# Kernel tuning notes

Measured on AMD Instinct MI355X. Metric: run time of the kernel, lower is better.

## Reference

```python
import jax, jax.numpy as jnp
import numpy as np

N = 50000   # nodes
E = 600000  # edges (avg degree ~12)
R = 8       # num_relations = 2 * n_speakers**2, n_speakers=2
B = 32      # num_bases = args.batch_size
GD, H1, H2 = 128, 128, 128


def setup_inputs() -> dict:
    key = jax.random.key(0)
    ks = jax.random.split(key, 16)
    w = lambda k, shape: jax.random.normal(k, shape, jnp.float32) * 0.05
    return {
        "node_features": jax.random.normal(ks[0], (N, GD), jnp.float32),
        "edge_index": jax.random.randint(ks[1], (2, E), 0, N),
        "edge_norm": jax.random.uniform(ks[2], (E,), jnp.float32),
        "edge_type": jax.random.randint(ks[3], (E,), 0, R),
        "basis": w(ks[4], (B, GD, H1)),
        "comp": w(ks[5], (R, B)),
        "root": w(ks[6], (GD, H1)),
        "bias1": jnp.zeros((H1,), jnp.float32),
        "w_key": w(ks[7], (H1, H2)),
        "b_key": jnp.zeros((H2,), jnp.float32),
        "w_query": w(ks[8], (H1, H2)),
        "b_query": jnp.zeros((H2,), jnp.float32),
        "w_value": w(ks[9], (H1, H2)),
        "b_value": jnp.zeros((H2,), jnp.float32),
        "w_skip": w(ks[10], (H1, H2)),
        "b_skip": jnp.zeros((H2,), jnp.float32),
    }


def reference(node_features, edge_index, edge_norm, edge_type, basis, comp,
              root, bias1, w_key, b_key, w_query, b_query, w_value, b_value,
              w_skip, b_skip):
    n = node_features.shape[0]
    r = comp.shape[0]
    src, dst = edge_index[0], edge_index[1]

    # ---- RGCNConv (basis decomposition, per-relation mean aggregation) ----
    W = jnp.einsum('rb,bio->rio', comp, basis)            # [R, GD, H1]
    xW = jnp.einsum('ni,rio->rno', node_features, W)      # [R, N, H1]
    msg = xW[edge_type, src]                              # [E, H1]
    seg = edge_type * n + dst                             # combined (relation, dst) segment id
    agg = jax.ops.segment_sum(msg, seg, num_segments=r * n).reshape(r, n, -1)
    cnt = jax.ops.segment_sum(jnp.ones(msg.shape[0], jnp.float32), seg,
                              num_segments=r * n).reshape(r, n, 1)
    h = (agg / jnp.maximum(cnt, 1.0)).sum(0) + node_features @ root + bias1

    # ---- ResGatedGraphConv: sigmoid(k_i + q_j) * v_j, sum-aggregated + skip ----
    k = h @ w_key + b_key
    q = h @ w_query + b_query
    v = h @ w_value + b_value
    m = jax.nn.sigmoid(k[dst] + q[src]) * v[src]          # [E, H2]
    out = jax.ops.segment_sum(m, dst, num_segments=n) + h @ w_skip + b_skip
    return out
```

## Files before the change

kernel.cpp:

```cpp
#include <hip/hip_runtime.h>
#include <stdint.h>

#define GD 128
#define H1 128
#define H2 128
#define NBASES 32
#define NREL 8
#define KZ 1152

typedef __attribute__((ext_vector_type(8))) short bf16x8;
typedef __attribute__((ext_vector_type(4))) float f32x4;

static inline size_t align256(size_t x){ return (x + 255) & ~(size_t)255; }

__device__ __forceinline__ float bf2f(uint32_t u16){
  union { uint32_t u; float f; } c; c.u = (u16 & 0xffffu) << 16; return c.f;
}
__device__ __forceinline__ unsigned short f2bf(float f){
  union { float f; uint32_t u; } c; c.f = f;
  uint32_t u = c.u;
  u += 0x7fffu + ((u >> 16) & 1u);
  return (unsigned short)(u >> 16);
}
__device__ __forceinline__ uint32_t pkbf(float a, float b){
  union { float f; uint32_t u; } ca, cb; ca.f = a; cb.f = b;
  return __builtin_amdgcn_perm(cb.u + 0x8000u, ca.u + 0x8000u, 0x07060302u);
}

__device__ __forceinline__ void async_copy16(void* lds_dst, const void* gsrc){
  __builtin_amdgcn_global_load_lds(
      (const __attribute__((address_space(1))) uint32_t*)gsrc,
      (__attribute__((address_space(3))) uint32_t*)lds_dst, 16, 0, 0);
}

__global__ void k_prep(const float* __restrict__ comp, const float* __restrict__ basis,
                       const float* __restrict__ root, unsigned short* __restrict__ Bz,
                       const float* __restrict__ wk, const float* __restrict__ wq,
                       const float* __restrict__ wv, const float* __restrict__ wsk,
                       const float* __restrict__ bk, const float* __restrict__ bq,
                       const float* __restrict__ bv, const float* __restrict__ bs,
                       unsigned short* __restrict__ B2t, float* __restrict__ Bb,
                       const float4* __restrict__ x, uint2* __restrict__ xout, int cnt4,
                       uint32_t* __restrict__ xpadz, int npadz,
                       const int* __restrict__ edst, const int* __restrict__ etyp,
                       int* __restrict__ cnt, int E, int n){
  int b = blockIdx.x, t = threadIdx.x;
  if (b < 576){
    int idx = b*256 + t;
    int row = idx >> 7, i = idx & 127;
    int r = row >> 7, o = row & 127;
    float v;
    if (r < 8){
      float acc = 0.f;
      #pragma unroll
      for (int bb = 0; bb < NBASES; ++bb)
        acc += comp[r*NBASES + bb] * basis[((size_t)bb*GD + i)*H1 + o];
      v = acc;
    } else {
      v = root[(size_t)i*H1 + o];
    }
    Bz[idx] = f2bf(v);
  } else if (b < 576 + 256){
    int idx = (b - 576)*256 + t;
    int c = idx / H1, k = idx % H1;
    const float* w = (c < 128) ? wk : (c < 256) ? wq : (c < 384) ? wv : wsk;
    B2t[idx] = f2bf(w[(size_t)k*H2 + (c & 127)]);
    if (idx < 512){
      const float* bia = (idx < 128) ? bk : (idx < 256) ? bq : (idx < 384) ? bv : bs;
      Bb[idx] = bia[idx & 127];
    }
  } else {
    int cb = b - (576 + 256);
    int ncastb = (cnt4 + 255) >> 8;
    if (cb < ncastb){
      int i = cb*256 + t;
      if (i < cnt4){
        float4 v = x[i];
        uint2 o; o.x = pkbf(v.x, v.y); o.y = pkbf(v.z, v.w);
        xout[i] = o;
      }
    } else if (cb < ncastb + 12){
      int i = (cb - ncastb)*256 + t;
      if (i < npadz) xpadz[i] = 0u;
    } else {
      int e = (cb - ncastb - 12)*256 + t;
      if (e < E) atomicAdd(&cnt[etyp[e]*n + edst[e]], 1);
    }
  }
}

__global__ void k_scanA(const int* __restrict__ deg, int* __restrict__ off,
                        int* __restrict__ btot, int len){
  __shared__ int wsum[16];
  int t = threadIdx.x, lane = t & 63, w = t >> 6;
  int i0 = blockIdx.x*8192 + t*8;
  int v[8];
  if (i0 + 7 < len){
    int4 va = *(const int4*)(deg + i0);
    int4 vb = *(const int4*)(deg + i0 + 4);
    v[0]=va.x; v[1]=va.y; v[2]=va.z; v[3]=va.w;
    v[4]=vb.x; v[5]=vb.y; v[6]=vb.z; v[7]=vb.w;
  } else {
    #pragma unroll
    for (int u = 0; u < 8; ++u) v[u] = (i0+u < len) ? deg[i0+u] : 0;
  }
  int s[8]; s[0] = v[0];
  #pragma unroll
  for (int u = 1; u < 8; ++u) s[u] = s[u-1] + v[u];
  int x = s[7];
  #pragma unroll
  for (int d = 1; d < 64; d <<= 1){
    int u = __shfl_up(x, d, 64);
    if (lane >= d) x += u;
  }
  if (lane == 63) wsum[w] = x;
  __syncthreads();
  if (t < 16){
    int y = wsum[t];
    #pragma unroll
    for (int d = 1; d < 16; d <<= 1){
      int u = __shfl_up(y, d, 16);
      if (t >= d) y += u;
    }
    wsum[t] = y;
  }
  __syncthreads();
  int woff = (w > 0) ? wsum[w-1] : 0;
  int excl = woff + x - s[7];
  #pragma unroll
  for (int u = 0; u < 8; ++u)
    if (i0+u < len) off[i0+u] = excl + s[u] - v[u];
  if (t == 0) btot[blockIdx.x] = wsum[15];
}

__global__ void k_scanB(const int* __restrict__ btot, int* __restrict__ off,
                        int* __restrict__ cursor, int len, int sentinel){
  int t = threadIdx.x, bid = blockIdx.x;
  int add = 0;
  for (int j = 0; j < bid; ++j) add += btot[j];
  int i0 = bid*8192 + t*8;
  #pragma unroll
  for (int u = 0; u < 8; ++u){
    int i = i0 + u;
    if (i < len){ int val = off[i] + add; off[i] = val; cursor[i] = val; }
  }
  if (bid == 0 && t == 0) off[len] = sentinel;
}

__global__ void k_scatter_rd(const int* __restrict__ src, const int* __restrict__ dst,
                             const int* __restrict__ typ, int* __restrict__ cursor,
                             int* __restrict__ pk, int E, int n){
  int e = blockIdx.x*blockDim.x + threadIdx.x;
  if (e >= E) return;
  int pos = atomicAdd(&cursor[typ[e]*n + dst[e]], 1);
  pk[pos] = src[e];
}

__launch_bounds__(256)
__global__ void k_zgemm(const unsigned short* __restrict__ A, const unsigned short* __restrict__ Bt,
                        unsigned short* __restrict__ Z){
  __shared__ char lds[16384];
  int t = threadIdx.x, lane = t & 63, wave = t >> 6;
  int row0 = blockIdx.x * 128;
  int c0 = blockIdx.y * 128;
  int mrow = lane & 15, quad = lane >> 4;
  int wrow = (wave & 1) * 64, wcol = (wave >> 1) * 64;
  int s = (mrow >> 1) & 3;

  const unsigned short* Asrc = A + (size_t)(row0 + (t >> 2))*H1 + (((t & 3) ^ ((t >> 3) & 3)) << 3);
  const unsigned short* Bsrc = Bt + (size_t)(c0 + (t >> 2))*H1 + (((t & 3) ^ ((t >> 3) & 3)) << 3);
  char* ldsw = lds + wave*1024;

  int aoff = (wrow + mrow)*64 + ((quad ^ s) << 4);
  int boff = 8192 + (wcol + mrow)*64 + ((quad ^ s) << 4);

  f32x4 acc[4][4];
  #pragma unroll
  for (int i = 0; i < 4; ++i)
    #pragma unroll
    for (int j = 0; j < 4; ++j) acc[i][j] = (f32x4){0.f,0.f,0.f,0.f};

  #pragma unroll
  for (int kt = 0; kt < H1; kt += 32){
    __syncthreads();
    async_copy16(ldsw,         Asrc + kt);
    async_copy16(ldsw + 4096,  Asrc + (size_t)64*H1 + kt);
    async_copy16(ldsw + 8192,  Bsrc + kt);
    async_copy16(ldsw + 12288, Bsrc + (size_t)64*H1 + kt);
    __syncthreads();
    bf16x8 af[4], bf[4];
    #pragma unroll
    for (int i = 0; i < 4; ++i) af[i] = *(const bf16x8*)(lds + aoff + i*1024);
    #pragma unroll
    for (int j = 0; j < 4; ++j) bf[j] = *(const bf16x8*)(lds + boff + j*1024);
    #pragma unroll
    for (int i = 0; i < 4; ++i)
      #pragma unroll
      for (int j = 0; j < 4; ++j)
        acc[i][j] = __builtin_amdgcn_mfma_f32_16x16x32_bf16(af[i], bf[j], acc[i][j], 0, 0, 0);
  }
  #pragma unroll
  for (int j = 0; j < 4; ++j){
    int col = c0 + wcol + j*16 + mrow;
    #pragma unroll
    for (int i = 0; i < 4; ++i)
      #pragma unroll
      for (int rg = 0; rg < 4; ++rg){
        int row = row0 + wrow + i*16 + quad*4 + rg;
        Z[(size_t)row*KZ + col] = f2bf(acc[i][j][rg]);
      }
  }
}

__global__ void k_edge1(const int* __restrict__ off_rd, const int* __restrict__ pk_rd,
                        const unsigned short* __restrict__ Zb,
                        const float* __restrict__ bias1,
                        unsigned short* __restrict__ h, int n, int npad){
  int wid = blockIdx.x*(blockDim.x >> 6) + (threadIdx.x >> 6);
  int lane = threadIdx.x & 63;
  if (wid >= npad) return;
  uint32_t* hrow = (uint32_t*)(h + (size_t)wid*H1);
  if (wid >= n){ hrow[lane] = 0u; return; }
  const uint32_t* Z32 = (const uint32_t*)Zb;
  int r8 = lane & 7;
  int o_r = off_rd[(size_t)r8*n + wid];
  int e_r = off_rd[(size_t)r8*n + wid + 1];
  int c_r = e_r - o_r;
  float ic_r = (c_r > 0) ? (1.f/(float)c_r) : 0.f;
  int c0_ = __builtin_amdgcn_readlane(c_r, 0), c1_ = __builtin_amdgcn_readlane(c_r, 1);
  int c2_ = __builtin_amdgcn_readlane(c_r, 2), c3_ = __builtin_amdgcn_readlane(c_r, 3);
  int c4_ = __builtin_amdgcn_readlane(c_r, 4), c5_ = __builtin_amdgcn_readlane(c_r, 5);
  int c6_ = __builtin_amdgcn_readlane(c_r, 6), c7_ = __builtin_amdgcn_readlane(c_r, 7);
  int o0_ = __builtin_amdgcn_readlane(o_r, 0), o1_ = __builtin_amdgcn_readlane(o_r, 1);
  int o2_ = __builtin_amdgcn_readlane(o_r, 2), o3_ = __builtin_amdgcn_readlane(o_r, 3);
  int o4_ = __builtin_amdgcn_readlane(o_r, 4), o5_ = __builtin_amdgcn_readlane(o_r, 5);
  int o6_ = __builtin_amdgcn_readlane(o_r, 6), o7_ = __builtin_amdgcn_readlane(o_r, 7);
  float i0f = __int_as_float(__builtin_amdgcn_readlane(__float_as_int(ic_r), 0));
  float i1f = __int_as_float(__builtin_amdgcn_readlane(__float_as_int(ic_r), 1));
  float i2f = __int_as_float(__builtin_amdgcn_readlane(__float_as_int(ic_r), 2));
  float i3f = __int_as_float(__builtin_amdgcn_readlane(__float_as_int(ic_r), 3));
  float i4f = __int_as_float(__builtin_amdgcn_readlane(__float_as_int(ic_r), 4));
  float i5f = __int_as_float(__builtin_amdgcn_readlane(__float_as_int(ic_r), 5));
  float i6f = __int_as_float(__builtin_amdgcn_readlane(__float_as_int(ic_r), 6));
  float i7f = __int_as_float(__builtin_amdgcn_readlane(__float_as_int(ic_r), 7));
  int p1 = c0_, p2 = p1 + c1_, p3 = p2 + c2_, p4 = p3 + c3_;
  int p5 = p4 + c4_, p6 = p5 + c5_, p7 = p6 + c6_, dg = p7 + c7_;

  float a0 = 0.f, a1 = 0.f;
  for (int jb = 0; jb < dg; jb += 64){
    int i = jb + lane;
    int adj = o0_, rel = 0;
    float wv = i0f;
    adj = (i >= p1) ? (o1_ - p1) : adj;  rel += (i >= p1);  wv = (i >= p1) ? i1f : wv;
    adj = (i >= p2) ? (o2_ - p2) : adj;  rel += (i >= p2);  wv = (i >= p2) ? i2f : wv;
    adj = (i >= p3) ? (o3_ - p3) : adj;  rel += (i >= p3);  wv = (i >= p3) ? i3f : wv;
    adj = (i >= p4) ? (o4_ - p4) : adj;  rel += (i >= p4);  wv = (i >= p4) ? i4f : wv;
    adj = (i >= p5) ? (o5_ - p5) : adj;  rel += (i >= p5);  wv = (i >= p5) ? i5f : wv;
    adj = (i >= p6) ? (o6_ - p6) : adj;  rel += (i >= p6);  wv = (i >= p6) ? i6f : wv;
    adj = (i >= p7) ? (o7_ - p7) : adj;  rel += (i >= p7);  wv = (i >= p7) ? i7f : wv;
    int m = dg - jb; if (m > 64) m = 64;
    int pj = (lane < m) ? pk_rd[adj + i] : 0;
    int gidx = pj*(KZ/2) + rel*64;
    int jj = 0;
    for (; jj + 8 <= m; jj += 8){
      uint32_t g[8]; float wgt[8];
      #pragma unroll
      for (int k = 0; k < 8; ++k){
        int gx = __builtin_amdgcn_readlane(gidx, jj + k);
        wgt[k] = __int_as_float(__builtin_amdgcn_readlane(__float_as_int(wv), jj + k));
        g[k] = Z32[(size_t)(uint32_t)gx + lane];
      }
      #pragma unroll
      for (int k = 0; k < 8; ++k){
        a0 += bf2f(g[k]) * wgt[k];
        a1 += bf2f(g[k] >> 16) * wgt[k];
      }
    }
    for (; jj + 4 <= m; jj += 4){
      uint32_t g[4]; float wgt[4];
      #pragma unroll
      for (int k = 0; k < 4; ++k){
        int gx = __builtin_amdgcn_readlane(gidx, jj + k);
        wgt[k] = __int_as_float(__builtin_amdgcn_readlane(__float_as_int(wv), jj + k));
        g[k] = Z32[(size_t)(uint32_t)gx + lane];
      }
      #pragma unroll
      for (int k = 0; k < 4; ++k){
        a0 += bf2f(g[k]) * wgt[k];
        a1 += bf2f(g[k] >> 16) * wgt[k];
      }
    }
    for (; jj < m; ++jj){
      int gx = __builtin_amdgcn_readlane(gidx, jj);
      float wg = __int_as_float(__builtin_amdgcn_readlane(__float_as_int(wv), jj));
      uint32_t gg = Z32[(size_t)(uint32_t)gx + lane];
      a0 += bf2f(gg) * wg;
      a1 += bf2f(gg >> 16) * wg;
    }
  }
  uint32_t zr = Z32[(size_t)wid*(KZ/2) + 512 + lane];
  float2 bb = ((const float2*)bias1)[lane];
  hrow[lane] = pkbf(a0 + bf2f(zr) + bb.x, a1 + bf2f(zr >> 16) + bb.y);
}

__launch_bounds__(256)
__global__ void k_gemm2(const unsigned short* __restrict__ A, const unsigned short* __restrict__ Bt,
                        const float* __restrict__ Bb, unsigned short* __restrict__ kqv,
                        unsigned short* __restrict__ skipb, int n){
  __shared__ char lds[16384];
  int t = threadIdx.x, lane = t & 63, wave = t >> 6;
  int row0 = blockIdx.x * 128;
  int c0 = blockIdx.y * 128;
  int mrow = lane & 15, quad = lane >> 4;
  int wrow = (wave & 1) * 64, wcol = (wave >> 1) * 64;
  int s = (mrow >> 1) & 3;

  const unsigned short* Asrc = A + (size_t)(row0 + (t >> 2))*H1 + (((t & 3) ^ ((t >> 3) & 3)) << 3);
  const unsigned short* Bsrc = Bt + (size_t)(c0 + (t >> 2))*H1 + (((t & 3) ^ ((t >> 3) & 3)) << 3);
  char* ldsw = lds + wave*1024;

  int aoff = (wrow + mrow)*64 + ((quad ^ s) << 4);
  int boff = 8192 + (wcol + mrow)*64 + ((quad ^ s) << 4);

  f32x4 acc[4][4];
  #pragma unroll
  for (int i = 0; i < 4; ++i)
    #pragma unroll
    for (int j = 0; j < 4; ++j) acc[i][j] = (f32x4){0.f,0.f,0.f,0.f};

  #pragma unroll
  for (int kt = 0; kt < H1; kt += 32){
    __syncthreads();
    async_copy16(ldsw,         Asrc + kt);
    async_copy16(ldsw + 4096,  Asrc + (size_t)64*H1 + kt);
    async_copy16(ldsw + 8192,  Bsrc + kt);
    async_copy16(ldsw + 12288, Bsrc + (size_t)64*H1 + kt);
    __syncthreads();
    bf16x8 af[4], bf[4];
    #pragma unroll
    for (int i = 0; i < 4; ++i) af[i] = *(const bf16x8*)(lds + aoff + i*1024);
    #pragma unroll
    for (int j = 0; j < 4; ++j) bf[j] = *(const bf16x8*)(lds + boff + j*1024);
    #pragma unroll
    for (int i = 0; i < 4; ++i)
      #pragma unroll
      for (int j = 0; j < 4; ++j)
        acc[i][j] = __builtin_amdgcn_mfma_f32_16x16x32_bf16(af[i], bf[j], acc[i][j], 0, 0, 0);
  }
  #pragma unroll
  for (int j = 0; j < 4; ++j){
    int col = c0 + wcol + j*16 + mrow;
    float bcol = Bb[col];
    #pragma unroll
    for (int i = 0; i < 4; ++i)
      #pragma unroll
      for (int rg = 0; rg < 4; ++rg){
        int rr = row0 + wrow + i*16 + quad*4 + rg;
        if (rr >= n) continue;
        float v = acc[i][j][rg] + bcol;
        if (col < 128){
          kqv[(size_t)rr*384 + col] = f2bf(v);
        } else if (col < 256){
          int jj = col - 128;
          kqv[(size_t)rr*384 + 128 + ((jj >> 1) << 2) + (jj & 1)] = f2bf(v);
        } else if (col < 384){
          int jj = col - 256;
          kqv[(size_t)rr*384 + 128 + ((jj >> 1) << 2) + 2 + (jj & 1)] = f2bf(v);
        } else {
          skipb[(size_t)rr*H2 + (col - 384)] = f2bf(v);
        }
      }
  }
}

__global__ void k_edge2(const int* __restrict__ off_rd, const int* __restrict__ pk_rd,
                        const unsigned short* __restrict__ kqv,
                        const unsigned short* __restrict__ skipb,
                        float* __restrict__ out, int n){
  int wid = blockIdx.x*(blockDim.x >> 6) + (threadIdx.x >> 6);
  int lane = threadIdx.x & 63;
  if (wid >= n) return;
  const uint32_t* kv32 = (const uint32_t*)kqv;
  int r = lane & 7;
  int o_r = off_rd[(size_t)r*n + wid];
  int e_r = off_rd[(size_t)r*n + wid + 1];
  int c_r = e_r - o_r;
  int c0_ = __builtin_amdgcn_readlane(c_r, 0), c1_ = __builtin_amdgcn_readlane(c_r, 1);
  int c2_ = __builtin_amdgcn_readlane(c_r, 2), c3_ = __builtin_amdgcn_readlane(c_r, 3);
  int c4_ = __builtin_amdgcn_readlane(c_r, 4), c5_ = __builtin_amdgcn_readlane(c_r, 5);
  int c6_ = __builtin_amdgcn_readlane(c_r, 6), c7_ = __builtin_amdgcn_readlane(c_r, 7);
  int o0_ = __builtin_amdgcn_readlane(o_r, 0), o1_ = __builtin_amdgcn_readlane(o_r, 1);
  int o2_ = __builtin_amdgcn_readlane(o_r, 2), o3_ = __builtin_amdgcn_readlane(o_r, 3);
  int o4_ = __builtin_amdgcn_readlane(o_r, 4), o5_ = __builtin_amdgcn_readlane(o_r, 5);
  int o6_ = __builtin_amdgcn_readlane(o_r, 6), o7_ = __builtin_amdgcn_readlane(o_r, 7);
  int p1 = c0_, p2 = p1 + c1_, p3 = p2 + c2_, p4 = p3 + c3_;
  int p5 = p4 + c4_, p6 = p5 + c5_, p7 = p6 + c6_, dg = p7 + c7_;

  uint32_t ku = kv32[(size_t)wid*192 + lane];
  float k0 = bf2f(ku), k1 = bf2f(ku >> 16);
  float a0 = 0.f, a1 = 0.f;
  for (int jb = 0; jb < dg; jb += 64){
    int i = jb + lane;
    int adj = o0_;
    adj = (i >= p1) ? (o1_ - p1) : adj;
    adj = (i >= p2) ? (o2_ - p2) : adj;
    adj = (i >= p3) ? (o3_ - p3) : adj;
    adj = (i >= p4) ? (o4_ - p4) : adj;
    adj = (i >= p5) ? (o5_ - p5) : adj;
    adj = (i >= p6) ? (o6_ - p6) : adj;
    adj = (i >= p7) ? (o7_ - p7) : adj;
    int m = dg - jb; if (m > 64) m = 64;
    int pj = (lane < m) ? pk_rd[adj + i] : 0;
    int jj = 0;
    for (; jj + 8 <= m; jj += 8){
      uint2 q[8];
      #pragma unroll
      for (int k = 0; k < 8; ++k){
        int s = __builtin_amdgcn_readlane(pj, jj + k);
        q[k] = *(const uint2*)(kv32 + (size_t)s*192 + 64 + lane*2);
      }
      #pragma unroll
      for (int k = 0; k < 8; ++k){
        float qq0 = bf2f(q[k].x), qq1 = bf2f(q[k].x >> 16);
        float vv0 = bf2f(q[k].y), vv1 = bf2f(q[k].y >> 16);
        float g0 = 1.f / (1.f + __expf(-(k0 + qq0)));
        float g1 = 1.f / (1.f + __expf(-(k1 + qq1)));
        a0 += g0*vv0; a1 += g1*vv1;
      }
    }
    for (; jj + 4 <= m; jj += 4){
      uint2 q[4];
      #pragma unroll
      for (int k = 0; k < 4; ++k){
        int s = __builtin_amdgcn_readlane(pj, jj + k);
        q[k] = *(const uint2*)(kv32 + (size_t)s*192 + 64 + lane*2);
      }
      #pragma unroll
      for (int k = 0; k < 4; ++k){
        float qq0 = bf2f(q[k].x), qq1 = bf2f(q[k].x >> 16);
        float vv0 = bf2f(q[k].y), vv1 = bf2f(q[k].y >> 16);
        float g0 = 1.f / (1.f + __expf(-(k0 + qq0)));
        float g1 = 1.f / (1.f + __expf(-(k1 + qq1)));
        a0 += g0*vv0; a1 += g1*vv1;
      }
    }
    for (; jj < m; ++jj){
      int s = __builtin_amdgcn_readlane(pj, jj);
      uint2 qc = *(const uint2*)(kv32 + (size_t)s*192 + 64 + lane*2);
      float qq0 = bf2f(qc.x), qq1 = bf2f(qc.x >> 16);
      float vv0 = bf2f(qc.y), vv1 = bf2f(qc.y >> 16);
      float g0 = 1.f / (1.f + __expf(-(k0 + qq0)));
      float g1 = 1.f / (1.f + __expf(-(k1 + qq1)));
      a0 += g0*vv0; a1 += g1*vv1;
    }
  }
  uint32_t sk = ((const uint32_t*)skipb)[(size_t)wid*64 + lane];
  float2 cur; cur.x = a0 + bf2f(sk); cur.y = a1 + bf2f(sk >> 16);
  ((float2*)(out + (size_t)wid*H2))[lane] = cur;
}

extern "C" void kernel_launch(void* const* d_in, const int* in_sizes, int n_in,
                              void* d_out, int out_size, void* d_ws, size_t ws_size,
                              hipStream_t stream){
  const float* x     = (const float*)d_in[0];
  const int*   eidx  = (const int*)  d_in[1];
  const int*   etype = (const int*)  d_in[3];
  const float* basis = (const float*)d_in[4];
  const float* comp  = (const float*)d_in[5];
  const float* root  = (const float*)d_in[6];
  const float* bias1 = (const float*)d_in[7];
  const float* wk    = (const float*)d_in[8];
  const float* bk    = (const float*)d_in[9];
  const float* wq    = (const float*)d_in[10];
  const float* bq    = (const float*)d_in[11];
  const float* wv    = (const float*)d_in[12];
  const float* bv    = (const float*)d_in[13];
  const float* wsk   = (const float*)d_in[14];
  const float* bs    = (const float*)d_in[15];
  const int n = in_sizes[0] / GD;
  const int E = in_sizes[3];
  const int npad = (n + 127) & ~127;
  const int* esrc = eidx;
  const int* edst = eidx + E;
  float* out = (float*)d_out;

  char* w = (char*)d_ws;
  size_t off = 0;
  unsigned short* xbf  = (unsigned short*)(w + off); off = align256(off + (size_t)npad*GD*2);
  unsigned short* Zbuf = (unsigned short*)(w + off); off = align256(off + (size_t)npad*KZ*2);
  unsigned short* Bz   = (unsigned short*)(w + off); off = align256(off + (size_t)KZ*H1*2);
  unsigned short* B2t  = (unsigned short*)(w + off); off = align256(off + (size_t)512*H1*2);
  float* Bb            = (float*)(w + off);          off = align256(off + 512*4);
  unsigned short* hbuf = (unsigned short*)(w + off); off = align256(off + (size_t)npad*H1*2);
  unsigned short* kqv  = (unsigned short*)(w + off); off = align256(off + (size_t)n*384*2);
  unsigned short* skipb= (unsigned short*)(w + off); off = align256(off + (size_t)npad*H2*2);
  int* cnt_rd          = (int*)(w + off);            off = align256(off + (size_t)(8*n+4)*4);
  int* off_rd          = (int*)(w + off);            off = align256(off + (size_t)(8*n+1)*4);
  int* cur_rd          = (int*)(w + off);            off = align256(off + (size_t)8*n*4);
  int* btot_rd         = (int*)(w + off);            off = align256(off + 64*4);
  int* pk_rd           = (int*)(w + off);            off = align256(off + (size_t)E*4);

  const int nblk_rd = (8*n + 8191) / 8192;
  const int cnt4 = n*GD/4;
  const int ncastb = (cnt4 + 255)/256;
  const int histb  = (E + 255)/256;
  const int npadz  = (npad - n)*GD/2;

  hipMemsetAsync(cnt_rd, 0, (size_t)8*n*4, stream);

  k_prep<<<576 + 256 + ncastb + 12 + histb, 256, 0, stream>>>(
      comp, basis, root, Bz, wk, wq, wv, wsk, bk, bq, bv, bs, B2t, Bb,
      (const float4*)x, (uint2*)xbf, cnt4,
      (uint32_t*)(xbf + (size_t)n*GD), npadz,
      edst, etype, cnt_rd, E, n);
  k_scanA<<<nblk_rd, 1024, 0, stream>>>(cnt_rd, off_rd, btot_rd, 8*n);
  k_scanB<<<nblk_rd, 1024, 0, stream>>>(btot_rd, off_rd, cur_rd, 8*n, E);
  k_scatter_rd<<<(E + 255)/256, 256, 0, stream>>>(esrc, edst, etype, cur_rd, pk_rd, E, n);
  k_zgemm<<<dim3(npad/128, KZ/128), 256, 0, stream>>>(xbf, Bz, Zbuf);
  k_edge1<<<(npad + 3)/4, 256, 0, stream>>>(off_rd, pk_rd, Zbuf, bias1, hbuf, n, npad);
  k_gemm2<<<dim3(npad/128, 4), 256, 0, stream>>>(hbuf, B2t, Bb, kqv, skipb, n);
  k_edge2<<<(n + 3)/4, 256, 0, stream>>>(off_rd, pk_rd, kqv, skipb, out, n);
}
```

Measured before the change: 379.2 us.

## Replace relation-by-destination CSR with destination-only CSR packing relation in index

Builds a CSR keyed only by destination node instead of by (relation, destination), with the edge's relation packed into the high bits of the source index. The scan shrinks from 8n to n entries and becomes a single-block serial-carry scan, so one kernel launch is removed. Per-relation counts are now recomputed inside edge1 with wave ballots instead of being read from eight offset arrays. The tradeoff is a single-block scan over n entries and extra ballot work per node. It also assumes node ids fit in 20 bits.

New measurement: 411.9 us. +8.6%, slower.

```diff
diff --git a/kernel.cpp b/kernel.cpp
--- a/kernel.cpp
+++ b/kernel.cpp
@@ -42,8 +42,7 @@
                        unsigned short* __restrict__ B2t, float* __restrict__ Bb,
                        const float4* __restrict__ x, uint2* __restrict__ xout, int cnt4,
                        uint32_t* __restrict__ xpadz, int npadz,
-                       const int* __restrict__ edst, const int* __restrict__ etyp,
-                       int* __restrict__ cnt, int E, int n){
+                       const int* __restrict__ edst, int* __restrict__ cnt, int E){
   int b = blockIdx.x, t = threadIdx.x;
   if (b < 576){
     int idx = b*256 + t;
@@ -84,76 +83,74 @@
       if (i < npadz) xpadz[i] = 0u;
     } else {
       int e = (cb - ncastb - 12)*256 + t;
-      if (e < E) atomicAdd(&cnt[etyp[e]*n + edst[e]], 1);
-    }
-  }
-}
-
-__global__ void k_scanA(const int* __restrict__ deg, int* __restrict__ off,
-                        int* __restrict__ btot, int len){
+      if (e < E) atomicAdd(&cnt[edst[e]], 1);
+    }
+  }
+}
+
+__global__ void k_scan1(const int* __restrict__ deg, int* __restrict__ off,
+                        int* __restrict__ cursor, int n, int E){
   __shared__ int wsum[16];
+  __shared__ int carry_s;
   int t = threadIdx.x, lane = t & 63, w = t >> 6;
-  int i0 = blockIdx.x*8192 + t*8;
-  int v[8];
-  if (i0 + 7 < len){
-    int4 va = *(const int4*)(deg + i0);
-    int4 vb = *(const int4*)(deg + i0 + 4);
-    v[0]=va.x; v[1]=va.y; v[2]=va.z; v[3]=va.w;
-    v[4]=vb.x; v[5]=vb.y; v[6]=vb.z; v[7]=vb.w;
-  } else {
-    #pragma unroll
-    for (int u = 0; u < 8; ++u) v[u] = (i0+u < len) ? deg[i0+u] : 0;
-  }
-  int s[8]; s[0] = v[0];
-  #pragma unroll
-  for (int u = 1; u < 8; ++u) s[u] = s[u-1] + v[u];
-  int x = s[7];
-  #pragma unroll
-  for (int d = 1; d < 64; d <<= 1){
-    int u = __shfl_up(x, d, 64);
-    if (lane >= d) x += u;
-  }
-  if (lane == 63) wsum[w] = x;
+  if (t == 0) carry_s = 0;
   __syncthreads();
-  if (t < 16){
-    int y = wsum[t];
-    #pragma unroll
-    for (int d = 1; d < 16; d <<= 1){
-      int u = __shfl_up(y, d, 16);
-      if (t >= d) y += u;
-    }
-    wsum[t] = y;
-  }
-  __syncthreads();
-  int woff = (w > 0) ? wsum[w-1] : 0;
-  int excl = woff + x - s[7];
-  #pragma unroll
-  for (int u = 0; u < 8; ++u)
-    if (i0+u < len) off[i0+u] = excl + s[u] - v[u];
-  if (t == 0) btot[blockIdx.x] = wsum[15];
-}
-
-__global__ void k_scanB(const int* __restrict__ btot, int* __restrict__ off,
-                        int* __restrict__ cursor, int len, int sentinel){
-  int t = threadIdx.x, bid = blockIdx.x;
-  int add = 0;
-  for (int j = 0; j < bid; ++j) add += btot[j];
-  int i0 = bid*8192 + t*8;
-  #pragma unroll
-  for (int u = 0; u < 8; ++u){
-    int i = i0 + u;
-    if (i < len){ int val = off[i] + add; off[i] = val; cursor[i] = val; }
-  }
-  if (bid == 0 && t == 0) off[len] = sentinel;
-}
-
-__global__ void k_scatter_rd(const int* __restrict__ src, const int* __restrict__ dst,
-                             const int* __restrict__ typ, int* __restrict__ cursor,
-                             int* __restrict__ pk, int E, int n){
+  for (int base = 0; base < n; base += 8192){
+    int i0 = base + t*8;
+    int v[8];
+    if (i0 + 7 < n){
+      int4 va = *(const int4*)(deg + i0);
+      int4 vb = *(const int4*)(deg + i0 + 4);
+      v[0]=va.x; v[1]=va.y; v[2]=va.z; v[3]=va.w;
+      v[4]=vb.x; v[5]=vb.y; v[6]=vb.z; v[7]=vb.w;
+    } else {
+      #pragma unroll
+      for (int u = 0; u < 8; ++u) v[u] = (i0+u < n) ? deg[i0+u] : 0;
+    }
+    int s[8]; s[0] = v[0];
+    #pragma unroll
+    for (int u = 1; u < 8; ++u) s[u] = s[u-1] + v[u];
+    int x = s[7];
+    #pragma unroll
+    for (int d = 1; d < 64; d <<= 1){
+      int u = __shfl_up(x, d, 64);
+      if (lane >= d) x += u;
+    }
+    if (lane == 63) wsum[w] = x;
+    int carry = carry_s;
+    __syncthreads();
+    if (t < 16){
+      int y = wsum[t];
+      #pragma unroll
+      for (int d = 1; d < 16; d <<= 1){
+        int u = __shfl_up(y, d, 16);
+        if (t >= d) y += u;
+      }
+      wsum[t] = y;
+    }
+    __syncthreads();
+    int woff = (w > 0) ? wsum[w-1] : 0;
+    int total = wsum[15];
+    int excl = carry + woff + x - s[7];
+    #pragma unroll
+    for (int u = 0; u < 8; ++u){
+      int i = i0 + u;
+      if (i < n){ int val = excl + s[u] - v[u]; off[i] = val; cursor[i] = val; }
+    }
+    __syncthreads();
+    if (t == 0) carry_s = carry + total;
+    __syncthreads();
+  }
+  if (t == 0) off[n] = E;
+}
+
+__global__ void k_scatter_d(const int* __restrict__ src, const int* __restrict__ dst,
+                            const int* __restrict__ typ, int* __restrict__ cursor,
+                            int* __restrict__ pk, int E){
   int e = blockIdx.x*blockDim.x + threadIdx.x;
   if (e >= E) return;
-  int pos = atomicAdd(&cursor[typ[e]*n + dst[e]], 1);
-  pk[pos] = src[e];
+  int pos = atomicAdd(&cursor[dst[e]], 1);
+  pk[pos] = src[e] | (typ[e] << 20);
 }
 
 __launch_bounds__(256)
@@ -212,7 +209,7 @@
   }
 }
 
-__global__ void k_edge1(const int* __restrict__ off_rd, const int* __restrict__ pk_rd,
+__global__ void k_edge1(const int* __restrict__ off_d, const int* __restrict__ pk_d,
                         const unsigned short* __restrict__ Zb,
                         const float* __restrict__ bias1,
                         unsigned short* __restrict__ h, int n, int npad){
@@ -222,45 +219,26 @@
   uint32_t* hrow = (uint32_t*)(h + (size_t)wid*H1);
   if (wid >= n){ hrow[lane] = 0u; return; }
   const uint32_t* Z32 = (const uint32_t*)Zb;
-  int r8 = lane & 7;
-  int o_r = off_rd[(size_t)r8*n + wid];
-  int e_r = off_rd[(size_t)r8*n + wid + 1];
-  int c_r = e_r - o_r;
-  float ic_r = (c_r > 0) ? (1.f/(float)c_r) : 0.f;
-  int c0_ = __builtin_amdgcn_readlane(c_r, 0), c1_ = __builtin_amdgcn_readlane(c_r, 1);
-  int c2_ = __builtin_amdgcn_readlane(c_r, 2), c3_ = __builtin_amdgcn_readlane(c_r, 3);
-  int c4_ = __builtin_amdgcn_readlane(c_r, 4), c5_ = __builtin_amdgcn_readlane(c_r, 5);
-  int c6_ = __builtin_amdgcn_readlane(c_r, 6), c7_ = __builtin_amdgcn_readlane(c_r, 7);
-  int o0_ = __builtin_amdgcn_readlane(o_r, 0), o1_ = __builtin_amdgcn_readlane(o_r, 1);
-  int o2_ = __builtin_amdgcn_readlane(o_r, 2), o3_ = __builtin_amdgcn_readlane(o_r, 3);
-  int o4_ = __builtin_amdgcn_readlane(o_r, 4), o5_ = __builtin_amdgcn_readlane(o_r, 5);
-  int o6_ = __builtin_amdgcn_readlane(o_r, 6), o7_ = __builtin_amdgcn_readlane(o_r, 7);
-  float i0f = __int_as_float(__builtin_amdgcn_readlane(__float_as_int(ic_r), 0));
-  float i1f = __int_as_float(__builtin_amdgcn_readlane(__float_as_int(ic_r), 1));
-  float i2f = __int_as_float(__builtin_amdgcn_readlane(__float_as_int(ic_r), 2));
-  float i3f = __int_as_float(__builtin_amdgcn_readlane(__float_as_int(ic_r), 3));
-  float i4f = __int_as_float(__builtin_amdgcn_readlane(__float_as_int(ic_r), 4));
-  float i5f = __int_as_float(__builtin_amdgcn_readlane(__float_as_int(ic_r), 5));
-  float i6f = __int_as_float(__builtin_amdgcn_readlane(__float_as_int(ic_r), 6));
-  float i7f = __int_as_float(__builtin_amdgcn_readlane(__float_as_int(ic_r), 7));
-  int p1 = c0_, p2 = p1 + c1_, p3 = p2 + c2_, p4 = p3 + c3_;
-  int p5 = p4 + c4_, p6 = p5 + c5_, p7 = p6 + c6_, dg = p7 + c7_;
+  int ov = off_d[wid + (lane & 1)];
+  int o = __builtin_amdgcn_readlane(ov, 0);
+  int dg = __builtin_amdgcn_readlane(ov, 1) - o;
 
   float a0 = 0.f, a1 = 0.f;
-  for (int jb = 0; jb < dg; jb += 64){
-    int i = jb + lane;
-    int adj = o0_, rel = 0;
-    float wv = i0f;
-    adj = (i >= p1) ? (o1_ - p1) : adj;  rel += (i >= p1);  wv = (i >= p1) ? i1f : wv;
-    adj = (i >= p2) ? (o2_ - p2) : adj;  rel += (i >= p2);  wv = (i >= p2) ? i2f : wv;
-    adj = (i >= p3) ? (o3_ - p3) : adj;  rel += (i >= p3);  wv = (i >= p3) ? i3f : wv;
-    adj = (i >= p4) ? (o4_ - p4) : adj;  rel += (i >= p4);  wv = (i >= p4) ? i4f : wv;
-    adj = (i >= p5) ? (o5_ - p5) : adj;  rel += (i >= p5);  wv = (i >= p5) ? i5f : wv;
-    adj = (i >= p6) ? (o6_ - p6) : adj;  rel += (i >= p6);  wv = (i >= p6) ? i6f : wv;
-    adj = (i >= p7) ? (o7_ - p7) : adj;  rel += (i >= p7);  wv = (i >= p7) ? i7f : wv;
-    int m = dg - jb; if (m > 64) m = 64;
-    int pj = (lane < m) ? pk_rd[adj + i] : 0;
-    int gidx = pj*(KZ/2) + rel*64;
+  if (dg <= 64){
+    int m = dg;
+    int pj = (lane < m) ? pk_d[o + lane] : 0;
+    int rel = (pj >> 20) & 7;
+    int cr[8];
+    #pragma unroll
+    for (int r = 0; r < 8; ++r)
+      cr[r] = __popcll(__ballot(lane < m && rel == r));
+    float inv[8];
+    #pragma unroll
+    for (int r = 0; r < 8; ++r) inv[r] = (cr[r] > 0) ? 1.f/(float)cr[r] : 0.f;
+    float wv = inv[0];
+    #pragma unroll
+    for (int r = 1; r < 8; ++r) wv = (rel == r) ? inv[r] : wv;
+    int gidx = (pj & 0xFFFFF)*(KZ/2) + rel*64;
     int jj = 0;
     for (; jj + 8 <= m; jj += 8){
       uint32_t g[8]; float wgt[8];
@@ -296,6 +274,52 @@
       uint32_t gg = Z32[(size_t)(uint32_t)gx + lane];
       a0 += bf2f(gg) * wg;
       a1 += bf2f(gg >> 16) * wg;
+    }
+  } else {
+    int cr[8];
+    #pragma unroll
+    for (int r = 0; r < 8; ++r) cr[r] = 0;
+    for (int jb = 0; jb < dg; jb += 64){
+      int m = dg - jb; if (m > 64) m = 64;
+      int pj = (lane < m) ? pk_d[o + jb + lane] : 0;
+      int rel = (pj >> 20) & 7;
+      #pragma unroll
+      for (int r = 0; r < 8; ++r)
+        cr[r] += __popcll(__ballot(lane < m && rel == r));
+    }
+    float inv[8];
+    #pragma unroll
+    for (int r = 0; r < 8; ++r) inv[r] = (cr[r] > 0) ? 1.f/(float)cr[r] : 0.f;
+    for (int jb = 0; jb < dg; jb += 64){
+      int m = dg - jb; if (m > 64) m = 64;
+      int pj = (lane < m) ? pk_d[o + jb + lane] : 0;
+      int rel = (pj >> 20) & 7;
+      float wv = inv[0];
+      #pragma unroll
+      for (int r = 1; r < 8; ++r) wv = (rel == r) ? inv[r] : wv;
+      int gidx = (pj & 0xFFFFF)*(KZ/2) + rel*64;
+      int jj = 0;
+      for (; jj + 8 <= m; jj += 8){
+        uint32_t g[8]; float wgt[8];
+        #pragma unroll
+        for (int k = 0; k < 8; ++k){
+          int gx = __builtin_amdgcn_readlane(gidx, jj + k);
+          wgt[k] = __int_as_float(__builtin_amdgcn_readlane(__float_as_int(wv), jj + k));
+          g[k] = Z32[(size_t)(uint32_t)gx + lane];
+        }
+        #pragma unroll
+        for (int k = 0; k < 8; ++k){
+          a0 += bf2f(g[k]) * wgt[k];
+          a1 += bf2f(g[k] >> 16) * wgt[k];
+        }
+      }
+      for (; jj < m; ++jj){
+        int gx = __builtin_amdgcn_readlane(gidx, jj);
+        float wg = __int_as_float(__builtin_amdgcn_readlane(__float_as_int(wv), jj));
+        uint32_t gg = Z32[(size_t)(uint32_t)gx + lane];
+        a0 += bf2f(gg) * wg;
+        a1 += bf2f(gg >> 16) * wg;
+      }
     }
   }
   uint32_t zr = Z32[(size_t)wid*(KZ/2) + 512 + lane];
@@ -373,7 +397,7 @@
   }
 }
 
-__global__ void k_edge2(const int* __restrict__ off_rd, const int* __restrict__ pk_rd,
+__global__ void k_edge2(const int* __restrict__ off_d, const int* __restrict__ pk_d,
                         const unsigned short* __restrict__ kqv,
                         const unsigned short* __restrict__ skipb,
                         float* __restrict__ out, int n){
@@ -381,42 +405,22 @@
   int lane = threadIdx.x & 63;
   if (wid >= n) return;
   const uint32_t* kv32 = (const uint32_t*)kqv;
-  int r = lane & 7;
-  int o_r = off_rd[(size_t)r*n + wid];
-  int e_r = off_rd[(size_t)r*n + wid + 1];
-  int c_r = e_r - o_r;
-  int c0_ = __builtin_amdgcn_readlane(c_r, 0), c1_ = __builtin_amdgcn_readlane(c_r, 1);
-  int c2_ = __builtin_amdgcn_readlane(c_r, 2), c3_ = __builtin_amdgcn_readlane(c_r, 3);
-  int c4_ = __builtin_amdgcn_readlane(c_r, 4), c5_ = __builtin_amdgcn_readlane(c_r, 5);
-  int c6_ = __builtin_amdgcn_readlane(c_r, 6), c7_ = __builtin_amdgcn_readlane(c_r, 7);
-  int o0_ = __builtin_amdgcn_readlane(o_r, 0), o1_ = __builtin_amdgcn_readlane(o_r, 1);
-  int o2_ = __builtin_amdgcn_readlane(o_r, 2), o3_ = __builtin_amdgcn_readlane(o_r, 3);
-  int o4_ = __builtin_amdgcn_readlane(o_r, 4), o5_ = __builtin_amdgcn_readlane(o_r, 5);
-  int o6_ = __builtin_amdgcn_readlane(o_r, 6), o7_ = __builtin_amdgcn_readlane(o_r, 7);
-  int p1 = c0_, p2 = p1 + c1_, p3 = p2 + c2_, p4 = p3 + c3_;
-  int p5 = p4 + c4_, p6 = p5 + c5_, p7 = p6 + c6_, dg = p7 + c7_;
+  int ov = off_d[wid + (lane & 1)];
+  int o = __builtin_amdgcn_readlane(ov, 0);
+  int dg = __builtin_amdgcn_readlane(ov, 1) - o;
 
   uint32_t ku = kv32[(size_t)wid*192 + lane];
   float k0 = bf2f(ku), k1 = bf2f(ku >> 16);
   float a0 = 0.f, a1 = 0.f;
   for (int jb = 0; jb < dg; jb += 64){
-    int i = jb + lane;
-    int adj = o0_;
-    adj = (i >= p1) ? (o1_ - p1) : adj;
-    adj = (i >= p2) ? (o2_ - p2) : adj;
-    adj = (i >= p3) ? (o3_ - p3) : adj;
-    adj = (i >= p4) ? (o4_ - p4) : adj;
-    adj = (i >= p5) ? (o5_ - p5) : adj;
-    adj = (i >= p6) ? (o6_ - p6) : adj;
-    adj = (i >= p7) ? (o7_ - p7) : adj;
     int m = dg - jb; if (m > 64) m = 64;
-    int pj = (lane < m) ? pk_rd[adj + i] : 0;
+    int pj = (lane < m) ? pk_d[o + jb + lane] : 0;
     int jj = 0;
     for (; jj + 8 <= m; jj += 8){
       uint2 q[8];
       #pragma unroll
       for (int k = 0; k < 8; ++k){
-        int s = __builtin_amdgcn_readlane(pj, jj + k);
+        int s = __builtin_amdgcn_readlane(pj, jj + k) & 0xFFFFF;
         q[k] = *(const uint2*)(kv32 + (size_t)s*192 + 64 + lane*2);
       }
       #pragma unroll
@@ -432,7 +436,7 @@
       uint2 q[4];
       #pragma unroll
       for (int k = 0; k < 4; ++k){
-        int s = __builtin_amdgcn_readlane(pj, jj + k);
+        int s = __builtin_amdgcn_readlane(pj, jj + k) & 0xFFFFF;
         q[k] = *(const uint2*)(kv32 + (size_t)s*192 + 64 + lane*2);
       }
       #pragma unroll
@@ -445,7 +449,7 @@
       }
     }
     for (; jj < m; ++jj){
-      int s = __builtin_amdgcn_readlane(pj, jj);
+      int s = __builtin_amdgcn_readlane(pj, jj) & 0xFFFFF;
       uint2 qc = *(const uint2*)(kv32 + (size_t)s*192 + 64 + lane*2);
       float qq0 = bf2f(qc.x), qq1 = bf2f(qc.x >> 16);
       float vv0 = bf2f(qc.y), vv1 = bf2f(qc.y >> 16);
@@ -494,30 +498,27 @@
   unsigned short* hbuf = (unsigned short*)(w + off); off = align256(off + (size_t)npad*H1*2);
   unsigned short* kqv  = (unsigned short*)(w + off); off = align256(off + (size_t)n*384*2);
   unsigned short* skipb= (unsigned short*)(w + off); off = align256(off + (size_t)npad*H2*2);
-  int* cnt_rd          = (int*)(w + off);            off = align256(off + (size_t)(8*n+4)*4);
-  int* off_rd          = (int*)(w + off);            off = align256(off + (size_t)(8*n+1)*4);
-  int* cur_rd          = (int*)(w + off);            off = align256(off + (size_t)8*n*4);
-  int* btot_rd         = (int*)(w + off);            off = align256(off + 64*4);
-  int* pk_rd           = (int*)(w + off);            off = align256(off + (size_t)E*4);
-
-  const int nblk_rd = (8*n + 8191) / 8192;
+  int* cnt_d           = (int*)(w + off);            off = align256(off + (size_t)(n+4)*4);
+  int* off_d           = (int*)(w + off);            off = align256(off + (size_t)(n+1)*4);
+  int* cur_d           = (int*)(w + off);            off = align256(off + (size_t)n*4);
+  int* pk_d            = (int*)(w + off);            off = align256(off + (size_t)E*4);
+
   const int cnt4 = n*GD/4;
   const int ncastb = (cnt4 + 255)/256;
   const int histb  = (E + 255)/256;
   const int npadz  = (npad - n)*GD/2;
 
-  hipMemsetAsync(cnt_rd, 0, (size_t)8*n*4, stream);
+  hipMemsetAsync(cnt_d, 0, (size_t)n*4, stream);
 
   k_prep<<<576 + 256 + ncastb + 12 + histb, 256, 0, stream>>>(
       comp, basis, root, Bz, wk, wq, wv, wsk, bk, bq, bv, bs, B2t, Bb,
       (const float4*)x, (uint2*)xbf, cnt4,
       (uint32_t*)(xbf + (size_t)n*GD), npadz,
-      edst, etype, cnt_rd, E, n);
-  k_scanA<<<nblk_rd, 1024, 0, stream>>>(cnt_rd, off_rd, btot_rd, 8*n);
-  k_scanB<<<nblk_rd, 1024, 0, stream>>>(btot_rd, off_rd, cur_rd, 8*n, E);
-  k_scatter_rd<<<(E + 255)/256, 256, 0, stream>>>(esrc, edst, etype, cur_rd, pk_rd, E, n);
+      edst, cnt_d, E);
+  k_scan1<<<1, 1024, 0, stream>>>(cnt_d, off_d, cur_d, n, E);
+  k_scatter_d<<<(E + 255)/256, 256, 0, stream>>>(esrc, edst, etype, cur_d, pk_d, E);
   k_zgemm<<<dim3(npad/128, KZ/128), 256, 0, stream>>>(xbf, Bz, Zbuf);
-  k_edge1<<<(npad + 3)/4, 256, 0, stream>>>(off_rd, pk_rd, Zbuf, bias1, hbuf, n, npad);
+  k_edge1<<<(npad + 3)/4, 256, 0, stream>>>(off_d, pk_d, Zbuf, bias1, hbuf, n, npad);
   k_gemm2<<<dim3(npad/128, 4), 256, 0, stream>>>(hbuf, B2t, Bb, kqv, skipb, n);
-  k_edge2<<<(n + 3)/4, 256, 0, stream>>>(off_rd, pk_rd, kqv, skipb, out, n);
-}
+  k_edge2<<<(n + 3)/4, 256, 0, stream>>>(off_d, pk_d, kqv, skipb, out, n);
+}
```
